# Performance work log

Measured on AMD Instinct MI355X. Metric: run time of the kernel, lower is better.

The kernel has to match this reference:

```python
import jax, jax.numpy as jnp
import numpy as np

# subgraph partition for subgraph_num == 7 (from sort_subgraph)
GRAPH_LIST = [5, 9, 9, 25, 9, 9, 12]  # sums to 78 nodes
B = 131072
EMB = 5
HID = 10


def setup_inputs() -> dict:
    key = jax.random.key(0)
    k1, k2 = jax.random.split(key)
    x = jax.random.normal(k1, (B, sum(GRAPH_LIST), EMB), dtype=jnp.float32)
    stdv = 1.0 / np.sqrt(EMB)  # matches reset_parameters (uniform(-stdv, stdv))
    weight = jax.random.uniform(k2, (EMB, HID), dtype=jnp.float32, minval=-stdv, maxval=stdv)
    return {"x": x, "weight": weight}


def reference(x, weight):
    # x: [B, 78, 5], weight: [5, 10] -> coarsen_features: [B, 7, 5]
    outs = []
    idx = 0
    for L in GRAPH_LIST:  # small fixed structural loop (7 subgraphs)
        sub = x[:, idx:idx + L]                      # [b, j, g]
        fw = jnp.einsum('bjg,gh->bjh', sub, weight)  # [b, j, h]
        # sum_i (fw_j . fw_i) == fw_j . sum_i fw_i  (same math as matrix+row-sum)
        scores = jnp.einsum('bjh,bh->bj', fw, fw.sum(axis=1))  # [b, j]
        att = jax.nn.softmax(scores, axis=1)          # softmax over nodes j
        pooled = jnp.einsum('bj,bjg->bg', att, sub)   # [b, g]
        outs.append(pooled[:, None, :])
        idx += L
    return jnp.concatenate(outs, axis=1)              # [b, 7, 5]
```

## Files before the change

### kernel.cpp

```cpp
#include <hip/hip_runtime.h>


static __device__ __forceinline__ float xsum(float a) {
  a += __shfl_xor(a, 16, 64);
  a += __shfl_xor(a, 32, 64);
  return a;
}
static __device__ __forceinline__ float xmax(float a) {
  a = fmaxf(a, __shfl_xor(a, 16, 64));
  a = fmaxf(a, __shfl_xor(a, 32, 64));
  return a;
}

template<int L, int SEGOFF, int OUTOFF>
__device__ __forceinline__ void seg64(const float* __restrict__ bp, int q,
                                      const float (&Mt)[15],
                                      float* __restrict__ ob) {
  constexpr int T[5][5] = {{0, 1, 2, 3, 4},  {1, 5, 6, 7, 8},
                           {2, 6, 9, 10, 11}, {3, 7, 10, 12, 13},
                           {4, 8, 11, 13, 14}};
  constexpr int NJ = (L + 3) / 4;
  const bool lastv = (q + 4 * (NJ - 1)) < L;

  float s[NJ][5];
#pragma unroll
  for (int k = 0; k < NJ; ++k) {
    int j = q + 4 * k;
    if (j > L - 1) j = L - 1;
#pragma unroll
    for (int g = 0; g < 5; ++g) s[k][g] = bp[SEGOFF + j * 5 + g];
  }
#pragma unroll
  for (int g = 0; g < 5; ++g) s[NJ - 1][g] = lastv ? s[NJ - 1][g] : 0.f;

  float ssl[5];
#pragma unroll
  for (int g = 0; g < 5; ++g) {
    float a = s[0][g];
#pragma unroll
    for (int k = 1; k < NJ; ++k) a += s[k][g];
    ssl[g] = xsum(a);
  }

  float v[5];
#pragma unroll
  for (int g = 0; g < 5; ++g) {
    float a = Mt[T[g][0]] * ssl[0];
#pragma unroll
    for (int h = 1; h < 5; ++h) a += Mt[T[g][h]] * ssl[h];
    v[g] = a;
  }

  float sc[NJ];
#pragma unroll
  for (int k = 0; k < NJ; ++k) {
    float a = s[k][0] * v[0];
#pragma unroll
    for (int g = 1; g < 5; ++g) a += s[k][g] * v[g];
    sc[k] = a;
  }
  sc[NJ - 1] = lastv ? sc[NJ - 1] : -3.0e38f;

  float ml = sc[0];
#pragma unroll
  for (int k = 1; k < NJ; ++k) ml = fmaxf(ml, sc[k]);
  float m = xmax(ml);

  float d = 0.f, pl[5] = {0.f, 0.f, 0.f, 0.f, 0.f};
#pragma unroll
  for (int k = 0; k < NJ; ++k) {
    float e = __expf(sc[k] - m);
    d += e;
#pragma unroll
    for (int g = 0; g < 5; ++g) pl[g] += e * s[k][g];
  }
  d = xsum(d);
  float inv = 1.0f / d;
#pragma unroll
  for (int g = 0; g < 5; ++g) pl[g] = xsum(pl[g]);
  if (q == 0) {
#pragma unroll
    for (int g = 0; g < 5; ++g) ob[OUTOFF + g] = pl[g] * inv;
  }
}

__global__ __launch_bounds__(256, 2) void meso_kernel(
    const float* __restrict__ x, const float* __restrict__ w,
    float* __restrict__ out) {
  __shared__ __align__(16) float4 sm4[3400];
  float* smf = (float*)sm4;
  const int t = threadIdx.x;
  const int wv = t >> 6, ln = t & 63, q = ln >> 4, r = ln & 15;
  const size_t blk = blockIdx.x;
  const float4* xp4 = (const float4*)x + blk * 24960;
  float4* o4 = (float4*)out + blk * 2240;

  float4 A0, A1, A2, A3, A4, A5, A6 = make_float4(0, 0, 0, 0);
  float4 B0, B1, B2, B3, B4, B5, B6 = make_float4(0, 0, 0, 0);

#define ISSUE(R, c)                                                    \
  { const float4* g_ = xp4 + (size_t)(c) * 1560;                       \
    R##0 = g_[t];        R##1 = g_[t + 256];  R##2 = g_[t + 512];      \
    R##3 = g_[t + 768];  R##4 = g_[t + 1024]; R##5 = g_[t + 1280];     \
    if (t >= 232) R##6 = g_[1304 + t]; }

#define WRITE(R, b)                                                    \
  { float4* l_ = sm4 + (b) * 1560;                                     \
    l_[t] = R##0;        l_[t + 256] = R##1;  l_[t + 512] = R##2;      \
    l_[t + 768] = R##3;  l_[t + 1024] = R##4; l_[t + 1280] = R##5;     \
    if (t >= 232) l_[1304 + t] = R##6; }

#define WAITC(n03, n3)                                                 \
  { if (wv == 3) asm volatile("s_waitcnt vmcnt(" #n3 ")" ::: "memory");\
    else         asm volatile("s_waitcnt vmcnt(" #n03 ")" ::: "memory"); }

#define BAR()                                                          \
  { asm volatile("s_waitcnt lgkmcnt(0)" ::: "memory");                 \
    __builtin_amdgcn_s_barrier();                                      \
    __builtin_amdgcn_sched_barrier(0); }

#define FLUSH(pp)                                                      \
  { if (ln < 35)                                                       \
      o4[(size_t)(pp) * 140 + wv * 35 + ln] =                          \
          sm4[3120 + ((pp) & 1) * 140 + wv * 35 + ln]; }

#define COMPUTE(par)                                                   \
  { const float* bp = smf + (par) * 6240 + r * 390;                    \
    float* ob = smf + 12480 + (par) * 560 + r * 35;                    \
    if (wv == 0) { seg64<25, 115, 15>(bp, q, Mt, ob); }                \
    else if (wv == 1) { seg64<12, 330, 30>(bp, q, Mt, ob);             \
                        seg64<5,  0,   0 >(bp, q, Mt, ob); }           \
    else if (wv == 2) { seg64<9,  25,  5 >(bp, q, Mt, ob);             \
                        seg64<9,  70,  10>(bp, q, Mt, ob); }           \
    else              { seg64<9,  240, 20>(bp, q, Mt, ob);             \
                        seg64<9,  285, 25>(bp, q, Mt, ob); } }

  ISSUE(A, 0)
  ISSUE(B, 1)

  float Mt[15];
  {
    int i = 0;
#pragma unroll
    for (int g = 0; g < 5; ++g)
#pragma unroll
      for (int h = g; h < 5; ++h, ++i) {
        float a = 0.f;
#pragma unroll
        for (int k = 0; k < 10; ++k) a += w[g * 10 + k] * w[h * 10 + k];
        Mt[i] = a;
      }
  }

  WAITC(6, 7)
  WRITE(A, 0)
  BAR()

#pragma unroll 1
  for (int p = 0; p < 16; p += 2) {
    if (p > 0) FLUSH(p - 1)
    if (p + 2 < 16) ISSUE(A, p + 2)
    COMPUTE(0)
    if (p == 0)       WAITC(6, 7)
    else if (p < 14)  WAITC(7, 8)
    else              WAITC(1, 1)
    WRITE(B, 1)
    BAR()

    FLUSH(p)
    if (p + 3 < 16) ISSUE(B, p + 3)
    COMPUTE(1)
    if (p + 2 < 16) {
      if (p + 1 < 14) WAITC(7, 8)
      else            WAITC(1, 1)
      WRITE(A, 0)
    }
    BAR()
  }
  FLUSH(15)
}

extern "C" void kernel_launch(void* const* d_in, const int* in_sizes, int n_in,
                              void* d_out, int out_size, void* d_ws, size_t ws_size,
                              hipStream_t stream) {
  const float* x = (const float*)d_in[0];
  const float* w = (const float*)d_in[1];
  float* out = (float*)d_out;
  int B = in_sizes[0] / 390;
  int grid = B / 256;
  meso_kernel<<<grid, 256, 0, stream>>>(x, w, out);
}
```

Measured before the change: 47.25 us.

## Deepen global load prefetch to three register buffers with fully unrolled phases

Adds a third register staging set so three chunks of x are in flight at once instead of two, and replaces the two-step loop with fifteen fully unrolled phases that have hand-tuned vmcnt wait counts. The goal is to hide more HBM latency behind the shared-memory compute. In exchange it holds seven more float4 registers per thread, which could cause spills or hurt occupancy under launch_bounds(256,2), and the hardcoded waitcnt values must match the exact instruction order the compiler emits.

```diff
diff --git a/kernel.cpp b/kernel.cpp
--- a/kernel.cpp
+++ b/kernel.cpp
@@ -97,6 +97,7 @@
 
   float4 A0, A1, A2, A3, A4, A5, A6 = make_float4(0, 0, 0, 0);
   float4 B0, B1, B2, B3, B4, B5, B6 = make_float4(0, 0, 0, 0);
+  float4 C0, C1, C2, C3, C4, C5, C6 = make_float4(0, 0, 0, 0);
 
 #define ISSUE(R, c)                                                    \
   { const float4* g_ = xp4 + (size_t)(c) * 1560;                       \
@@ -135,8 +136,20 @@
     else              { seg64<9,  240, 20>(bp, q, Mt, ob);             \
                         seg64<9,  285, 25>(bp, q, Mt, ob); } }
 
+#define PHASE(k, Ri, Rw, n03, n3)                                      \
+  {                                                                    \
+    if ((k) > 0) FLUSH((k) - 1)                                        \
+    if ((k) <= 12) ISSUE(Ri, (k) + 3)                                  \
+    __builtin_amdgcn_sched_barrier(0);                                 \
+    COMPUTE((k) & 1)                                                   \
+    WAITC(n03, n3)                                                     \
+    WRITE(Rw, ((k) + 1) & 1)                                           \
+    BAR()                                                              \
+  }
+
   ISSUE(A, 0)
   ISSUE(B, 1)
+  ISSUE(C, 2)
 
   float Mt[15];
   {
@@ -152,31 +165,30 @@
       }
   }
 
-  WAITC(6, 7)
+  WAITC(12, 14)
   WRITE(A, 0)
   BAR()
 
-#pragma unroll 1
-  for (int p = 0; p < 16; p += 2) {
-    if (p > 0) FLUSH(p - 1)
-    if (p + 2 < 16) ISSUE(A, p + 2)
-    COMPUTE(0)
-    if (p == 0)       WAITC(6, 7)
-    else if (p < 14)  WAITC(7, 8)
-    else              WAITC(1, 1)
-    WRITE(B, 1)
-    BAR()
-
-    FLUSH(p)
-    if (p + 3 < 16) ISSUE(B, p + 3)
-    COMPUTE(1)
-    if (p + 2 < 16) {
-      if (p + 1 < 14) WAITC(7, 8)
-      else            WAITC(1, 1)
-      WRITE(A, 0)
-    }
-    BAR()
-  }
+  PHASE(0,  A, B, 12, 14)
+  PHASE(1,  B, C, 13, 15)
+  PHASE(2,  C, A, 14, 16)
+  PHASE(3,  A, B, 14, 16)
+  PHASE(4,  B, C, 14, 16)
+  PHASE(5,  C, A, 14, 16)
+  PHASE(6,  A, B, 14, 16)
+  PHASE(7,  B, C, 14, 16)
+  PHASE(8,  C, A, 14, 16)
+  PHASE(9,  A, B, 14, 16)
+  PHASE(10, B, C, 14, 16)
+  PHASE(11, C, A, 14, 16)
+  PHASE(12, A, B, 14, 16)
+  PHASE(13, B, C, 8,  9)
+  PHASE(14, C, A, 2,  2)
+
+  FLUSH(14)
+  COMPUTE(1)
+  asm volatile("s_waitcnt lgkmcnt(0)" ::: "memory");
+  __builtin_amdgcn_s_barrier();
   FLUSH(15)
 }
 
```

After: 52.87 us. 1.12x slower.

## Triple-buffer LDS chunks so staging writes and loads run ahead of compute

Applied to the files above, without the earlier changes.

Shared memory grows from two to three input chunk buffers plus output staging. Each step now writes the next chunk into a spare buffer and issues the following global load before computing the current chunk, so register-held loads drain earlier and more global traffic overlaps compute. The scheduling barrier after each block barrier is also removed, letting the compiler move instructions across it. The cost is a larger LDS footprint, close to the per-CU limit for two blocks, and more complex prologue and epilogue code with hand-tuned vmcnt waits.

```diff
diff --git a/kernel.cpp b/kernel.cpp
--- a/kernel.cpp
+++ b/kernel.cpp
@@ -87,8 +87,8 @@
 __global__ __launch_bounds__(256, 2) void meso_kernel(
     const float* __restrict__ x, const float* __restrict__ w,
     float* __restrict__ out) {
-  __shared__ __align__(16) float4 sm4[3400];
-  float* smf = (float*)sm4;
+  __shared__ __align__(16) float smf[19840];
+  float4* sm4 = (float4*)smf;
   const int t = threadIdx.x;
   const int wv = t >> 6, ln = t & 63, q = ln >> 4, r = ln & 15;
   const size_t blk = blockIdx.x;
@@ -104,8 +104,8 @@
     R##3 = g_[t + 768];  R##4 = g_[t + 1024]; R##5 = g_[t + 1280];     \
     if (t >= 232) R##6 = g_[1304 + t]; }
 
-#define WRITE(R, b)                                                    \
-  { float4* l_ = sm4 + (b) * 1560;                                     \
+#define WRITE(R, bi)                                                   \
+  { float4* l_ = sm4 + (bi) * 1560;                                    \
     l_[t] = R##0;        l_[t + 256] = R##1;  l_[t + 512] = R##2;      \
     l_[t + 768] = R##3;  l_[t + 1024] = R##4; l_[t + 1280] = R##5;     \
     if (t >= 232) l_[1304 + t] = R##6; }
@@ -116,17 +116,16 @@
 
 #define BAR()                                                          \
   { asm volatile("s_waitcnt lgkmcnt(0)" ::: "memory");                 \
-    __builtin_amdgcn_s_barrier();                                      \
-    __builtin_amdgcn_sched_barrier(0); }
+    __builtin_amdgcn_s_barrier(); }
 
 #define FLUSH(pp)                                                      \
   { if (ln < 35)                                                       \
       o4[(size_t)(pp) * 140 + wv * 35 + ln] =                          \
-          sm4[3120 + ((pp) & 1) * 140 + wv * 35 + ln]; }
-
-#define COMPUTE(par)                                                   \
-  { const float* bp = smf + (par) * 6240 + r * 390;                    \
-    float* ob = smf + 12480 + (par) * 560 + r * 35;                    \
+          sm4[4680 + ((pp) & 1) * 140 + wv * 35 + ln]; }
+
+#define COMPUTE(cb, outp)                                              \
+  { const float* bp = smf + (cb) * 6240 + r * 390;                     \
+    float* ob = smf + 18720 + (outp) * 560 + r * 35;                   \
     if (wv == 0) { seg64<25, 115, 15>(bp, q, Mt, ob); }                \
     else if (wv == 1) { seg64<12, 330, 30>(bp, q, Mt, ob);             \
                         seg64<5,  0,   0 >(bp, q, Mt, ob); }           \
@@ -154,29 +153,54 @@
 
   WAITC(6, 7)
   WRITE(A, 0)
-  BAR()
-
+  ISSUE(A, 2)
+  BAR()
+
+  WAITC(6, 7)
+  WRITE(B, 1)
+  ISSUE(B, 3)
+  COMPUTE(0, 0)
+  BAR()
+
+  FLUSH(0)
+  WAITC(7, 8)
+  WRITE(A, 2)
+  ISSUE(A, 4)
+  COMPUTE(1, 1)
+  BAR()
+
+  int cbE = 2;
 #pragma unroll 1
-  for (int p = 0; p < 16; p += 2) {
-    if (p > 0) FLUSH(p - 1)
-    if (p + 2 < 16) ISSUE(A, p + 2)
-    COMPUTE(0)
-    if (p == 0)       WAITC(6, 7)
-    else if (p < 14)  WAITC(7, 8)
-    else              WAITC(1, 1)
-    WRITE(B, 1)
+  for (int p = 2; p < 14; p += 2) {
+    int wbE = cbE + 1; if (wbE >= 3) wbE -= 3;
+    int wbO = cbE + 2; if (wbO >= 3) wbO -= 3;
+
+    FLUSH(p - 1)
+    WAITC(8, 9)
+    WRITE(B, wbE)
+    if (p + 3 < 16) ISSUE(B, p + 3)
+    COMPUTE(cbE, 0)
     BAR()
 
     FLUSH(p)
-    if (p + 3 < 16) ISSUE(B, p + 3)
-    COMPUTE(1)
-    if (p + 2 < 16) {
-      if (p + 1 < 14) WAITC(7, 8)
-      else            WAITC(1, 1)
-      WRITE(A, 0)
-    }
+    WAITC(8, 9)
+    WRITE(A, wbO)
+    if (p + 4 < 16) ISSUE(A, p + 4)
+    COMPUTE(wbE, 1)
     BAR()
-  }
+
+    cbE = wbO;
+  }
+
+  FLUSH(13)
+  WAITC(2, 2)
+  WRITE(B, 0)
+  COMPUTE(2, 0)
+  BAR()
+
+  FLUSH(14)
+  COMPUTE(0, 1)
+  BAR()
   FLUSH(15)
 }
 
```

Measured after the change: 48.57 us. 1.03x slower.
